# Kernel optimization log

Hardware: AMD Instinct MI355X
Metric: run time of the kernel (lower is better)

Reference implementation:

```python
import jax, jax.numpy as jnp
import numpy as np
import math

B, S, D, L, H, V, MAXP = 8, 512, 1024, 6, 8, 32000, 4096
HD = D // H
FF = 4 * D
EPS = 1e-5
SCALE = 1.0 / math.sqrt(HD)


def _ln(x, g, b):
    m = x.mean(-1, keepdims=True)
    xm = x - m
    v = (xm * xm).mean(-1, keepdims=True)
    return xm * jax.lax.rsqrt(v + EPS) * g + b


def setup_inputs() -> dict:
    key = jax.random.key(0)
    ks = jax.random.split(key, 16)
    std = 0.02
    inp = {
        'input_ids': jax.random.randint(ks[0], (B, S), 0, V, dtype=jnp.int32),
        'attention_mask': jnp.ones((B, S), dtype=jnp.int32),
        'current_position': 0,
        'tok_emb': jax.random.normal(ks[1], (V, D), jnp.float32) * std,
        'pos_emb': jax.random.normal(ks[2], (MAXP, D), jnp.float32) * std,
        'ln1_s': jnp.ones((L, D), jnp.float32),
        'ln1_b': jnp.zeros((L, D), jnp.float32),
        'Wq': jax.random.normal(ks[3], (L, D, D), jnp.float32) * std,
        'bq': jnp.zeros((L, D), jnp.float32),
        'Wk': jax.random.normal(ks[4], (L, D, D), jnp.float32) * std,
        'bk': jnp.zeros((L, D), jnp.float32),
        'Wv': jax.random.normal(ks[5], (L, D, D), jnp.float32) * std,
        'bv': jnp.zeros((L, D), jnp.float32),
        'Wo': jax.random.normal(ks[6], (L, D, D), jnp.float32) * std,
        'bo': jnp.zeros((L, D), jnp.float32),
        'ln2_s': jnp.ones((L, D), jnp.float32),
        'ln2_b': jnp.zeros((L, D), jnp.float32),
        'W1': jax.random.normal(ks[7], (L, D, FF), jnp.float32) * std,
        'b1': jnp.zeros((L, FF), jnp.float32),
        'W2': jax.random.normal(ks[8], (L, FF, D), jnp.float32) * std,
        'b2': jnp.zeros((L, D), jnp.float32),
        'lnf_s': jnp.ones((D,), jnp.float32),
        'lnf_b': jnp.zeros((D,), jnp.float32),
        'Wout': jax.random.normal(ks[9], (D, D), jnp.float32) * std,
        'bout': jnp.zeros((D,), jnp.float32),
    }
    return inp


def reference(input_ids, attention_mask, current_position, tok_emb, pos_emb,
              ln1_s, ln1_b, Wq, bq, Wk, bk, Wv, bv, Wo, bo,
              ln2_s, ln2_b, W1, b1, W2, b2, lnf_s, lnf_b, Wout, bout):
    pos = current_position + jnp.arange(S)  # [S]
    h = tok_emb[input_ids] + pos_emb[pos][None, :, :]  # [B,S,D]
    pad = (attention_mask == 0)[:, None, None, :]  # [B,1,1,S] key-padding mask

    def layer(h, p):
        (l1s, l1b, wq, bq_, wk, bk_, wv, bv_, wo, bo_,
         l2s, l2b, w1, b1_, w2, b2_) = p
        x = _ln(h, l1s, l1b)
        q = (x @ wq + bq_).reshape(B, S, H, HD).transpose(0, 2, 1, 3)
        k = (x @ wk + bk_).reshape(B, S, H, HD).transpose(0, 2, 1, 3)
        v = (x @ wv + bv_).reshape(B, S, H, HD).transpose(0, 2, 1, 3)
        scores = jnp.einsum('bhqd,bhkd->bhqk', q, k) * SCALE
        scores = jnp.where(pad, -10000.0, scores)
        attn = jax.nn.softmax(scores, axis=-1)
        o = jnp.einsum('bhqk,bhkd->bhqd', attn, v)
        o = o.transpose(0, 2, 1, 3).reshape(B, S, D)
        h = h + (o @ wo + bo_)
        x = _ln(h, l2s, l2b)
        mlp = jax.nn.gelu(x @ w1 + b1_, approximate=False) @ w2 + b2_
        return h + mlp, None

    h, _ = jax.lax.scan(layer, h, (ln1_s, ln1_b, Wq, bq, Wk, bk, Wv, bv, Wo, bo,
                                   ln2_s, ln2_b, W1, b1, W2, b2))
    h = _ln(h, lnf_s, lnf_b)
    return h @ Wout + bout
```

## Files before the change

kernel.cpp:

```cpp
#include <hip/hip_runtime.h>
#include <hip/hip_bf16.h>
#include <math.h>

#define BB 8
#define SS 512
#define DD 1024
#define LL 6
#define HH 8
#define HDD 128
#define FFF 4096
#define EPSF 1e-5f
#define SCALEF 0.08838834764831845f

typedef __attribute__((ext_vector_type(8))) _Float16 f16x8;
typedef __attribute__((ext_vector_type(4))) _Float16 f16x4;
typedef __attribute__((ext_vector_type(4))) float f32x4;

__device__ __forceinline__ void gload16(const void* g, void* l) {
  __builtin_amdgcn_global_load_lds(
      (const __attribute__((address_space(1))) void*)g,
      (__attribute__((address_space(3))) void*)l, 16, 0, 0);
}

__global__ __launch_bounds__(256, 3) void gemmk_kernel(
    const _Float16* __restrict__ Ag, const _Float16* __restrict__ Bg,
    const float* __restrict__ bias, void* __restrict__ outp,
    int Ndim, int Kdim, int Kstr, long zsA, long zsB, long zsOut, int emode) {
  __shared__ _Float16 lA[8192];
  __shared__ _Float16 lB[8192];
  const int tid = threadIdx.x;
  const int lane = tid & 63;
  const int wid = tid >> 6;
  const int z = blockIdx.z;
  const int m0 = blockIdx.y * 128;
  const int n0 = blockIdx.x * 128;
  const long K2 = (long)Kstr * 2;
  const _Float16* Az = Ag + (long)z * zsA + (long)m0 * Kstr;
  const _Float16* Bz = Bg + (long)z * zsB + (long)n0 * Kstr;

  const int wm = (wid >> 1) * 64;
  const int wn = (wid & 1) * 64;
  const int r16 = lane & 15;
  const int kq = lane >> 4;

  const char* As[4];
  const char* Bs[4];
  int ldd[4];
#pragma unroll
  for (int i = 0; i < 4; ++i) {
    const int idx = tid + i * 256;
    const int r = idx >> 3;
    const int sc = ((idx & 7) << 4) ^ ((r & 7) << 4);
    As[i] = (const char*)Az + (long)r * K2 + sc;
    Bs[i] = (const char*)Bz + (long)r * K2 + sc;
    ldd[i] = idx * 16;
  }

  f32x4 acc[4][4];
#pragma unroll
  for (int mi = 0; mi < 4; ++mi)
#pragma unroll
    for (int ni = 0; ni < 4; ++ni) acc[mi][ni] = (f32x4){0.f, 0.f, 0.f, 0.f};

  const int nt = Kdim >> 6;
  for (int t = 0; t < nt; ++t) {
    const int kb = t << 7;
    __syncthreads();
#pragma unroll
    for (int i = 0; i < 4; ++i) {
      gload16(As[i] + kb, (char*)lA + ldd[i]);
      gload16(Bs[i] + kb, (char*)lB + ldd[i]);
    }
    __syncthreads();
#pragma unroll
    for (int kk = 0; kk < 2; ++kk) {
      f16x8 af[4], bf[4];
#pragma unroll
      for (int mi = 0; mi < 4; ++mi) {
        const int R = wm + mi * 16 + r16;
        af[mi] = *(const f16x8*)((const char*)lA + R * 128 +
                                 ((kk * 64 + kq * 16) ^ ((R & 7) << 4)));
      }
#pragma unroll
      for (int ni = 0; ni < 4; ++ni) {
        const int R = wn + ni * 16 + r16;
        bf[ni] = *(const f16x8*)((const char*)lB + R * 128 +
                                 ((kk * 64 + kq * 16) ^ ((R & 7) << 4)));
      }
#pragma unroll
      for (int mi = 0; mi < 4; ++mi)
#pragma unroll
        for (int ni = 0; ni < 4; ++ni)
          acc[mi][ni] = __builtin_amdgcn_mfma_f32_16x16x32_f16(
              af[mi], bf[ni], acc[mi][ni], 0, 0, 0);
    }
  }

  _Float16* outH = (_Float16*)outp + (long)z * zsOut;
  const int rj = (lane >> 4) << 2;
  const long MSZq = (long)BB * SS * DD;
#pragma unroll
  for (int mi = 0; mi < 4; ++mi) {
#pragma unroll
    for (int ni = 0; ni < 4; ++ni) {
      const int col = n0 + wn + ni * 16 + r16;
#pragma unroll
      for (int j = 0; j < 4; ++j) {
        const int row = m0 + wm + mi * 16 + rj + j;
        float vv = acc[mi][ni][j];
        if (emode == 1) {
          vv += bias[col];
          int wsel = col >> 10, c = col & 1023;
          int b_ = row >> 9, s_ = row & 511;
          int hh = c >> 7, hd_ = c & 127;
          if (wsel < 2) {
            outH[wsel * MSZq + (((long)(b_ * HH + hh)) * SS + s_) * HDD + hd_] =
                (_Float16)vv;
          } else {
            outH[2 * MSZq + (((long)(b_ * HH + hh)) * HDD + hd_) * SS + s_] =
                (_Float16)vv;
          }
        } else if (emode == 5) {
          vv += bias[col];
          vv = 0.5f * vv * (1.0f + erff(vv * 0.70710678118654752f));
          outH[(long)row * Ndim + col] = (_Float16)vv;
        } else {
          outH[(long)row * Ndim + col] = (_Float16)vv;
        }
      }
    }
  }
}

__global__ __launch_bounds__(256) void flash_kernel(
    const _Float16* __restrict__ Qg, const _Float16* __restrict__ Kg,
    const _Float16* __restrict__ Vt, const int* __restrict__ amask,
    _Float16* __restrict__ xout) {
  __shared__ _Float16 Pl[4][32][136];
  __shared__ float rf_s[4][32];
  const int tid = threadIdx.x;
  const int lane = tid & 63;
  const int w = tid >> 6;
  const int bh = blockIdx.y;
  const int b_ = bh >> 3, hh = bh & 7;
  const int q0 = blockIdx.x * 128 + w * 32;
  const int r16 = lane & 15;
  const int kq = lane >> 4;
  const int rj = kq << 2;
  const _Float16* Qb = Qg + ((long)bh * SS + q0) * HDD;
  const _Float16* Kb = Kg + (long)bh * SS * HDD;
  const _Float16* Vb = Vt + (long)bh * HDD * SS;

  f16x8 qa[2][4];
#pragma unroll
  for (int mi = 0; mi < 2; ++mi)
#pragma unroll
    for (int kk = 0; kk < 4; ++kk)
      qa[mi][kk] = *(const f16x8*)(Qb + (long)(mi * 16 + r16) * HDD + kk * 32 +
                                   kq * 8);

  f32x4 acc[8][2];
#pragma unroll
  for (int mi = 0; mi < 8; ++mi)
#pragma unroll
    for (int ni = 0; ni < 2; ++ni) acc[mi][ni] = (f32x4){0.f, 0.f, 0.f, 0.f};
  float mrun[2][4], lrun[2][4];
#pragma unroll
  for (int mi = 0; mi < 2; ++mi)
#pragma unroll
    for (int j = 0; j < 4; ++j) {
      mrun[mi][j] = -INFINITY;
      lrun[mi][j] = 0.f;
    }

  for (int kt = 0; kt < 4; ++kt) {
    __syncthreads();
    const int s0 = kt * 128;
    int am[8];
#pragma unroll
    for (int ni = 0; ni < 8; ++ni)
      am[ni] = amask[b_ * SS + s0 + ni * 16 + r16];

    f32x4 sc[2][8];
#pragma unroll
    for (int mi = 0; mi < 2; ++mi)
#pragma unroll
      for (int ni = 0; ni < 8; ++ni) sc[mi][ni] = (f32x4){0.f, 0.f, 0.f, 0.f};
#pragma unroll
    for (int ni = 0; ni < 8; ++ni) {
      f16x8 kf[4];
#pragma unroll
      for (int kk = 0; kk < 4; ++kk)
        kf[kk] = *(const f16x8*)(Kb + (long)(s0 + ni * 16 + r16) * HDD +
                                 kk * 32 + kq * 8);
#pragma unroll
      for (int mi = 0; mi < 2; ++mi)
#pragma unroll
        for (int kk = 0; kk < 4; ++kk)
          sc[mi][ni] = __builtin_amdgcn_mfma_f32_16x16x32_f16(
              qa[mi][kk], kf[kk], sc[mi][ni], 0, 0, 0);
    }
#pragma unroll
    for (int mi = 0; mi < 2; ++mi)
#pragma unroll
      for (int ni = 0; ni < 8; ++ni)
#pragma unroll
        for (int j = 0; j < 4; ++j)
          sc[mi][ni][j] = am[ni] ? sc[mi][ni][j] * SCALEF : -10000.0f;

    float rf[2][4];
#pragma unroll
    for (int mi = 0; mi < 2; ++mi)
#pragma unroll
      for (int j = 0; j < 4; ++j) {
        float rm = -INFINITY;
#pragma unroll
        for (int ni = 0; ni < 8; ++ni) rm = fmaxf(rm, sc[mi][ni][j]);
#pragma unroll
        for (int off = 1; off < 16; off <<= 1)
          rm = fmaxf(rm, __shfl_xor(rm, off));
        const float mn = fmaxf(mrun[mi][j], rm);
        const float rfv = __expf(mrun[mi][j] - mn);
        mrun[mi][j] = mn;
        float rs = 0.f;
#pragma unroll
        for (int ni = 0; ni < 8; ++ni) {
          const float p = __expf(sc[mi][ni][j] - mn);
          sc[mi][ni][j] = p;
          rs += p;
        }
#pragma unroll
        for (int off = 1; off < 16; off <<= 1) rs += __shfl_xor(rs, off);
        lrun[mi][j] = lrun[mi][j] * rfv + rs;
        rf[mi][j] = rfv;
      }
    if (r16 == 0) {
#pragma unroll
      for (int mi = 0; mi < 2; ++mi)
#pragma unroll
        for (int j = 0; j < 4; ++j) rf_s[w][mi * 16 + rj + j] = rf[mi][j];
    }
#pragma unroll
    for (int mi = 0; mi < 2; ++mi)
#pragma unroll
      for (int ni = 0; ni < 8; ++ni)
#pragma unroll
        for (int j = 0; j < 4; ++j)
          Pl[w][mi * 16 + rj + j][ni * 16 + r16] = (_Float16)sc[mi][ni][j];
    __syncthreads();

    float rfq[2];
    rfq[0] = rf_s[w][r16];
    rfq[1] = rf_s[w][16 + r16];
#pragma unroll
    for (int mi2 = 0; mi2 < 8; ++mi2)
#pragma unroll
      for (int ni2 = 0; ni2 < 2; ++ni2)
#pragma unroll
        for (int j = 0; j < 4; ++j) acc[mi2][ni2][j] *= rfq[ni2];

    f16x8 pb[2][4];
#pragma unroll
    for (int ni2 = 0; ni2 < 2; ++ni2)
#pragma unroll
      for (int kk = 0; kk < 4; ++kk)
        pb[ni2][kk] =
            *(const f16x8*)(&Pl[w][ni2 * 16 + r16][kk * 32 + kq * 8]);
#pragma unroll
    for (int mi2 = 0; mi2 < 8; ++mi2) {
      f16x8 va[4];
#pragma unroll
      for (int kk = 0; kk < 4; ++kk)
        va[kk] = *(const f16x8*)(Vb + (long)(mi2 * 16 + r16) * SS + s0 +
                                 kk * 32 + kq * 8);
#pragma unroll
      for (int ni2 = 0; ni2 < 2; ++ni2)
#pragma unroll
        for (int kk = 0; kk < 4; ++kk)
          acc[mi2][ni2] = __builtin_amdgcn_mfma_f32_16x16x32_f16(
              va[kk], pb[ni2][kk], acc[mi2][ni2], 0, 0, 0);
    }
  }

  __syncthreads();
  if (r16 == 0) {
#pragma unroll
    for (int mi = 0; mi < 2; ++mi)
#pragma unroll
      for (int j = 0; j < 4; ++j)
        rf_s[w][mi * 16 + rj + j] = 1.0f / lrun[mi][j];
  }
  __syncthreads();
  float lq[2];
  lq[0] = rf_s[w][r16];
  lq[1] = rf_s[w][16 + r16];
#pragma unroll
  for (int mi2 = 0; mi2 < 8; ++mi2)
#pragma unroll
    for (int ni2 = 0; ni2 < 2; ++ni2) {
      f16x4 o;
#pragma unroll
      for (int j = 0; j < 4; ++j) o[j] = (_Float16)(acc[mi2][ni2][j] * lq[ni2]);
      const int qg = q0 + ni2 * 16 + r16;
      *(f16x4*)(&xout[((long)(b_ * SS + qg)) * DD + hh * HDD + mi2 * 16 + rj]) =
          o;
    }
}

__global__ __launch_bounds__(256) void reduce_ln_kernel(
    const _Float16* __restrict__ parts, int npart,
    const float* __restrict__ res, const float* __restrict__ bias,
    const float* __restrict__ lg, const float* __restrict__ lb,
    float* __restrict__ hout, _Float16* __restrict__ xout, long pzs) {
  const int row = blockIdx.x;
  const int c = threadIdx.x << 2;
  const long base = (long)row * DD + c;
  float4 a = *reinterpret_cast<const float4*>(&bias[c]);
  if (res) {
    const float4 r = *reinterpret_cast<const float4*>(&res[base]);
    a.x += r.x; a.y += r.y; a.z += r.z; a.w += r.w;
  }
  for (int p = 0; p < npart; ++p) {
    const f16x4 hpv = *reinterpret_cast<const f16x4*>(&parts[p * pzs + base]);
    a.x += (float)hpv[0]; a.y += (float)hpv[1];
    a.z += (float)hpv[2]; a.w += (float)hpv[3];
  }
  *reinterpret_cast<float4*>(&hout[base]) = a;
  if (!lg) return;
  float s = a.x + a.y + a.z + a.w;
  float ss = a.x * a.x + a.y * a.y + a.z * a.z + a.w * a.w;
#pragma unroll
  for (int off = 32; off; off >>= 1) {
    s += __shfl_down(s, off);
    ss += __shfl_down(ss, off);
  }
  __shared__ float red[8];
  const int wid = threadIdx.x >> 6, lane = threadIdx.x & 63;
  if (lane == 0) { red[wid] = s; red[4 + wid] = ss; }
  __syncthreads();
  if (threadIdx.x == 0) {
    s = red[0] + red[1] + red[2] + red[3];
    ss = red[4] + red[5] + red[6] + red[7];
    float mean = s * (1.0f / DD);
    float var = ss * (1.0f / DD) - mean * mean;
    red[0] = mean;
    red[1] = rsqrtf(var + EPSF);
  }
  __syncthreads();
  const float mean = red[0], rstd = red[1];
  const float4 gv = *reinterpret_cast<const float4*>(&lg[c]);
  const float4 bv = *reinterpret_cast<const float4*>(&lb[c]);
  f16x4 o;
  o[0] = (_Float16)((a.x - mean) * rstd * gv.x + bv.x);
  o[1] = (_Float16)((a.y - mean) * rstd * gv.y + bv.y);
  o[2] = (_Float16)((a.z - mean) * rstd * gv.z + bv.z);
  o[3] = (_Float16)((a.w - mean) * rstd * gv.w + bv.w);
  *reinterpret_cast<f16x4*>(&xout[base]) = o;
}

__global__ __launch_bounds__(256) void embed_ln_kernel(
    const int* __restrict__ ids, const int* __restrict__ curpos,
    const float* __restrict__ tok, const float* __restrict__ pos,
    const float* __restrict__ lg, const float* __restrict__ lb,
    float* __restrict__ h, _Float16* __restrict__ x) {
  const int rs = blockIdx.x;
  const int s_ = rs & (SS - 1);
  const int t = ids[rs];
  const int p = curpos[0] + s_;
  const int c = threadIdx.x << 2;
  const float4 tv = *reinterpret_cast<const float4*>(&tok[(long)t * DD + c]);
  const float4 pv = *reinterpret_cast<const float4*>(&pos[(long)p * DD + c]);
  float4 a = {tv.x + pv.x, tv.y + pv.y, tv.z + pv.z, tv.w + pv.w};
  *reinterpret_cast<float4*>(&h[(long)rs * DD + c]) = a;
  float s = a.x + a.y + a.z + a.w;
  float ss = a.x * a.x + a.y * a.y + a.z * a.z + a.w * a.w;
#pragma unroll
  for (int off = 32; off; off >>= 1) {
    s += __shfl_down(s, off);
    ss += __shfl_down(ss, off);
  }
  __shared__ float red[8];
  const int wid = threadIdx.x >> 6, lane = threadIdx.x & 63;
  if (lane == 0) { red[wid] = s; red[4 + wid] = ss; }
  __syncthreads();
  if (threadIdx.x == 0) {
    s = red[0] + red[1] + red[2] + red[3];
    ss = red[4] + red[5] + red[6] + red[7];
    float mean = s * (1.0f / DD);
    float var = ss * (1.0f / DD) - mean * mean;
    red[0] = mean;
    red[1] = rsqrtf(var + EPSF);
  }
  __syncthreads();
  const float mean = red[0], rstd = red[1];
  const float4 gv = *reinterpret_cast<const float4*>(&lg[c]);
  const float4 bv = *reinterpret_cast<const float4*>(&lb[c]);
  f16x4 o;
  o[0] = (_Float16)((a.x - mean) * rstd * gv.x + bv.x);
  o[1] = (_Float16)((a.y - mean) * rstd * gv.y + bv.y);
  o[2] = (_Float16)((a.z - mean) * rstd * gv.z + bv.z);
  o[3] = (_Float16)((a.w - mean) * rstd * gv.w + bv.w);
  *reinterpret_cast<f16x4*>(&x[(long)rs * DD + c]) = o;
}

__global__ __launch_bounds__(256) void wtransall_kernel(
    const float* __restrict__ Wq, const float* __restrict__ Wk,
    const float* __restrict__ Wv, const float* __restrict__ Wo,
    const float* __restrict__ W1, const float* __restrict__ W2, int l,
    _Float16* __restrict__ qkvT, _Float16* __restrict__ woT,
    _Float16* __restrict__ w1T, _Float16* __restrict__ w2T) {
  __shared__ float tt[64][65];
  const int id = blockIdx.x;
  const float* src;
  _Float16* dst;
  int K, N, t;
  const long lo = (long)l * DD * DD;
  const long lof = (long)l * DD * FFF;
  if (id < 1024) {
    const int wsel = id >> 8;
    t = id & 255;
    src = (wsel == 0 ? Wq : wsel == 1 ? Wk : wsel == 2 ? Wv : Wo) + lo;
    dst = (wsel < 3) ? (qkvT + (long)wsel * DD * DD) : woT;
    K = DD; N = DD;
  } else if (id < 2048) {
    t = id - 1024; src = W1 + lof; dst = w1T; K = DD; N = FFF;
  } else {
    t = id - 2048; src = W2 + lof; dst = w2T; K = FFF; N = DD;
  }
  const int ntile = N >> 6;
  const int n0 = (t % ntile) << 6;
  const int k0 = (t / ntile) << 6;
  const int tx = threadIdx.x & 63;
  const int ty = threadIdx.x >> 6;
#pragma unroll
  for (int i = 0; i < 16; ++i)
    tt[i * 4 + ty][tx] = src[(long)(k0 + i * 4 + ty) * N + n0 + tx];
  __syncthreads();
#pragma unroll
  for (int i = 0; i < 16; ++i) {
    const int r = i * 4 + ty;
    dst[(long)(n0 + r) * K + k0 + tx] = (_Float16)tt[tx][r];
  }
}

__global__ __launch_bounds__(256) void wtrans_kernel(
    const float* __restrict__ W, _Float16* __restrict__ WT, int K, int N) {
  __shared__ float tt[64][65];
  const int n0 = blockIdx.x * 64, k0 = blockIdx.y * 64;
  const int tx = threadIdx.x & 63;
  const int ty = threadIdx.x >> 6;
#pragma unroll
  for (int i = 0; i < 16; ++i)
    tt[i * 4 + ty][tx] = W[(long)(k0 + i * 4 + ty) * N + n0 + tx];
  __syncthreads();
#pragma unroll
  for (int i = 0; i < 16; ++i) {
    const int r = i * 4 + ty;
    WT[(long)(n0 + r) * K + k0 + tx] = (_Float16)tt[tx][r];
  }
}

__global__ __launch_bounds__(256) void packb_kernel(
    const float* __restrict__ bq, const float* __restrict__ bk,
    const float* __restrict__ bv, float* __restrict__ bqkv) {
  const int i = blockIdx.x * 256 + threadIdx.x;
  const int l = i / (3 * DD), j = i % (3 * DD);
  float v;
  if (j < DD) v = bq[l * DD + j];
  else if (j < 2 * DD) v = bk[l * DD + j - DD];
  else v = bv[l * DD + j - 2 * DD];
  bqkv[i] = v;
}

extern "C" void kernel_launch(void* const* d_in, const int* in_sizes, int n_in,
                              void* d_out, int out_size, void* d_ws,
                              size_t ws_size, hipStream_t stream) {
  const int* ids = (const int*)d_in[0];
  const int* amask = (const int*)d_in[1];
  const int* curp = (const int*)d_in[2];
  const float* tok = (const float*)d_in[3];
  const float* pose = (const float*)d_in[4];
  const float* ln1s = (const float*)d_in[5];
  const float* ln1b = (const float*)d_in[6];
  const float* Wq = (const float*)d_in[7];
  const float* bq = (const float*)d_in[8];
  const float* Wk = (const float*)d_in[9];
  const float* bk = (const float*)d_in[10];
  const float* Wv = (const float*)d_in[11];
  const float* bv = (const float*)d_in[12];
  const float* Wo = (const float*)d_in[13];
  const float* bo = (const float*)d_in[14];
  const float* ln2s = (const float*)d_in[15];
  const float* ln2b = (const float*)d_in[16];
  const float* W1 = (const float*)d_in[17];
  const float* b1 = (const float*)d_in[18];
  const float* W2 = (const float*)d_in[19];
  const float* b2 = (const float*)d_in[20];
  const float* lnfs = (const float*)d_in[21];
  const float* lnfb = (const float*)d_in[22];
  const float* Wout = (const float*)d_in[23];
  const float* bout = (const float*)d_in[24];

  const long MSZ = (long)BB * SS * DD;
  char* wsp = (char*)d_ws;
  float* h = (float*)wsp;
  _Float16* x = (_Float16*)(wsp + 16u * 1024 * 1024);
  _Float16* q = x + MSZ;
  _Float16* kb = q + MSZ;
  _Float16* vt = kb + MSZ;
  _Float16* big = vt + MSZ;
  _Float16* wqkvT = big + (long)BB * HH * SS * SS;
  _Float16* woT = wqkvT + 3L * DD * DD;
  _Float16* w1T = woT + (long)DD * DD;
  _Float16* w2T = w1T + (long)DD * FFF;
  float* bqkv = (float*)(w2T + (long)FFF * DD);
  _Float16* parts = (_Float16*)(bqkv + LL * 3 * DD);

  const int M = BB * SS;
  dim3 blk(256);
  const long pzs = (long)M * DD;

  embed_ln_kernel<<<M, blk, 0, stream>>>(ids, curp, tok, pose, ln1s, ln1b, h, x);
  packb_kernel<<<(LL * 3 * DD) / 256, blk, 0, stream>>>(bq, bk, bv, bqkv);

  const dim3 gQKV(3 * DD / 128, M / 128, 1);
  const dim3 gFA(SS / 128, BB * HH);
  const dim3 gF1(FFF / 128, M / 128, 1);
  const dim3 gK2(DD / 128, M / 128, 2);
  const dim3 gK4(DD / 128, M / 128, 4);
  const dim3 gWt(DD / 64, DD / 64);

  for (int l = 0; l < LL; ++l) {
    wtransall_kernel<<<3072, blk, 0, stream>>>(Wq, Wk, Wv, Wo, W1, W2, l,
                                               wqkvT, woT, w1T, w2T);
    gemmk_kernel<<<gQKV, blk, 0, stream>>>(x, wqkvT, bqkv + l * 3 * DD, q,
                                           3 * DD, DD, DD, 0, 0, 0, 1);
    flash_kernel<<<gFA, blk, 0, stream>>>(q, kb, vt, amask, x);
    gemmk_kernel<<<gK2, blk, 0, stream>>>(x, woT, nullptr, parts, DD, DD / 2,
                                          DD, DD / 2, DD / 2, pzs, 6);
    reduce_ln_kernel<<<M, blk, 0, stream>>>(parts, 2, h, bo + l * DD,
                                            ln2s + l * DD, ln2b + l * DD, h, x,
                                            pzs);
    gemmk_kernel<<<gF1, blk, 0, stream>>>(x, w1T, b1 + l * FFF, big, FFF, DD,
                                          DD, 0, 0, 0, 5);
    gemmk_kernel<<<gK4, blk, 0, stream>>>(big, w2T, nullptr, parts, DD,
                                          FFF / 4, FFF, FFF / 4, FFF / 4, pzs,
                                          6);
    const float* ng = (l < LL - 1) ? (ln1s + (l + 1) * DD) : lnfs;
    const float* nb = (l < LL - 1) ? (ln1b + (l + 1) * DD) : lnfb;
    reduce_ln_kernel<<<M, blk, 0, stream>>>(parts, 4, h, b2 + l * DD, ng, nb,
                                            h, x, pzs);
  }
  wtrans_kernel<<<gWt, blk, 0, stream>>>(Wout, woT, DD, DD);
  gemmk_kernel<<<gK2, blk, 0, stream>>>(x, woT, nullptr, parts, DD, DD / 2,
                                        DD, DD / 2, DD / 2, pzs, 6);
  reduce_ln_kernel<<<M, blk, 0, stream>>>(parts, 2, nullptr, bout, nullptr,
                                          nullptr, (float*)d_out, nullptr, pzs);
}
```

Measured before the change: 1.603 ms.

## Prepack all layer weights upfront, shrink flash tiles, split-K 4 for Wo

Transposes all six layers' weights into per-layer slabs with one launch up front when the workspace is large enough, instead of one transpose launch per layer. Flash attention now gives each wave 16 query rows instead of 32, which doubles the number of blocks and cuts register use. The Wo and output projections switch from split-K 2 to split-K 4, adding more partial sums for the reduce. The GEMM also raises its occupancy hint to 4 and recomputes load addresses to save registers. The risks are more K/V reloads per query row in attention and extra partial-sum traffic from the wider split-K.

New measurement: 1.732 ms. 1.08x slower.

```diff
diff --git a/kernel.cpp b/kernel.cpp
--- a/kernel.cpp
+++ b/kernel.cpp
@@ -22,7 +22,7 @@
       (__attribute__((address_space(3))) void*)l, 16, 0, 0);
 }
 
-__global__ __launch_bounds__(256, 3) void gemmk_kernel(
+__global__ __launch_bounds__(256, 4) void gemmk_kernel(
     const _Float16* __restrict__ Ag, const _Float16* __restrict__ Bg,
     const float* __restrict__ bias, void* __restrict__ outp,
     int Ndim, int Kdim, int Kstr, long zsA, long zsB, long zsOut, int emode) {
@@ -35,25 +35,21 @@
   const int m0 = blockIdx.y * 128;
   const int n0 = blockIdx.x * 128;
   const long K2 = (long)Kstr * 2;
-  const _Float16* Az = Ag + (long)z * zsA + (long)m0 * Kstr;
-  const _Float16* Bz = Bg + (long)z * zsB + (long)n0 * Kstr;
+  const char* Azc = (const char*)(Ag + (long)z * zsA + (long)m0 * Kstr);
+  const char* Bzc = (const char*)(Bg + (long)z * zsB + (long)n0 * Kstr);
 
   const int wm = (wid >> 1) * 64;
   const int wn = (wid & 1) * 64;
   const int r16 = lane & 15;
   const int kq = lane >> 4;
 
-  const char* As[4];
-  const char* Bs[4];
-  int ldd[4];
+  long roff[4];
 #pragma unroll
   for (int i = 0; i < 4; ++i) {
     const int idx = tid + i * 256;
     const int r = idx >> 3;
     const int sc = ((idx & 7) << 4) ^ ((r & 7) << 4);
-    As[i] = (const char*)Az + (long)r * K2 + sc;
-    Bs[i] = (const char*)Bz + (long)r * K2 + sc;
-    ldd[i] = idx * 16;
+    roff[i] = (long)r * K2 + sc;
   }
 
   f32x4 acc[4][4];
@@ -68,8 +64,8 @@
     __syncthreads();
 #pragma unroll
     for (int i = 0; i < 4; ++i) {
-      gload16(As[i] + kb, (char*)lA + ldd[i]);
-      gload16(Bs[i] + kb, (char*)lB + ldd[i]);
+      gload16(Azc + roff[i] + kb, (char*)lA + tid * 16 + i * 4096);
+      gload16(Bzc + roff[i] + kb, (char*)lB + tid * 16 + i * 4096);
     }
     __syncthreads();
 #pragma unroll
@@ -136,14 +132,14 @@
     const _Float16* __restrict__ Qg, const _Float16* __restrict__ Kg,
     const _Float16* __restrict__ Vt, const int* __restrict__ amask,
     _Float16* __restrict__ xout) {
-  __shared__ _Float16 Pl[4][32][136];
-  __shared__ float rf_s[4][32];
+  __shared__ _Float16 Pl[4][16][136];
+  __shared__ float rf_s[4][16];
   const int tid = threadIdx.x;
   const int lane = tid & 63;
   const int w = tid >> 6;
   const int bh = blockIdx.y;
   const int b_ = bh >> 3, hh = bh & 7;
-  const int q0 = blockIdx.x * 128 + w * 32;
+  const int q0 = blockIdx.x * 64 + w * 16;
   const int r16 = lane & 15;
   const int kq = lane >> 4;
   const int rj = kq << 2;
@@ -151,27 +147,20 @@
   const _Float16* Kb = Kg + (long)bh * SS * HDD;
   const _Float16* Vb = Vt + (long)bh * HDD * SS;
 
-  f16x8 qa[2][4];
-#pragma unroll
-  for (int mi = 0; mi < 2; ++mi)
-#pragma unroll
-    for (int kk = 0; kk < 4; ++kk)
-      qa[mi][kk] = *(const f16x8*)(Qb + (long)(mi * 16 + r16) * HDD + kk * 32 +
-                                   kq * 8);
-
-  f32x4 acc[8][2];
-#pragma unroll
-  for (int mi = 0; mi < 8; ++mi)
-#pragma unroll
-    for (int ni = 0; ni < 2; ++ni) acc[mi][ni] = (f32x4){0.f, 0.f, 0.f, 0.f};
-  float mrun[2][4], lrun[2][4];
-#pragma unroll
-  for (int mi = 0; mi < 2; ++mi)
-#pragma unroll
-    for (int j = 0; j < 4; ++j) {
-      mrun[mi][j] = -INFINITY;
-      lrun[mi][j] = 0.f;
-    }
+  f16x8 qa[4];
+#pragma unroll
+  for (int kk = 0; kk < 4; ++kk)
+    qa[kk] = *(const f16x8*)(Qb + (long)r16 * HDD + kk * 32 + kq * 8);
+
+  f32x4 acc[8];
+#pragma unroll
+  for (int mi = 0; mi < 8; ++mi) acc[mi] = (f32x4){0.f, 0.f, 0.f, 0.f};
+  float mrun[4], lrun[4];
+#pragma unroll
+  for (int j = 0; j < 4; ++j) {
+    mrun[j] = -INFINITY;
+    lrun[j] = 0.f;
+  }
 
   for (int kt = 0; kt < 4; ++kt) {
     __syncthreads();
@@ -181,11 +170,9 @@
     for (int ni = 0; ni < 8; ++ni)
       am[ni] = amask[b_ * SS + s0 + ni * 16 + r16];
 
-    f32x4 sc[2][8];
-#pragma unroll
-    for (int mi = 0; mi < 2; ++mi)
-#pragma unroll
-      for (int ni = 0; ni < 8; ++ni) sc[mi][ni] = (f32x4){0.f, 0.f, 0.f, 0.f};
+    f32x4 sc[8];
+#pragma unroll
+    for (int ni = 0; ni < 8; ++ni) sc[ni] = (f32x4){0.f, 0.f, 0.f, 0.f};
 #pragma unroll
     for (int ni = 0; ni < 8; ++ni) {
       f16x8 kf[4];
@@ -194,117 +181,89 @@
         kf[kk] = *(const f16x8*)(Kb + (long)(s0 + ni * 16 + r16) * HDD +
                                  kk * 32 + kq * 8);
 #pragma unroll
-      for (int mi = 0; mi < 2; ++mi)
-#pragma unroll
-        for (int kk = 0; kk < 4; ++kk)
-          sc[mi][ni] = __builtin_amdgcn_mfma_f32_16x16x32_f16(
-              qa[mi][kk], kf[kk], sc[mi][ni], 0, 0, 0);
-    }
-#pragma unroll
-    for (int mi = 0; mi < 2; ++mi)
-#pragma unroll
-      for (int ni = 0; ni < 8; ++ni)
-#pragma unroll
-        for (int j = 0; j < 4; ++j)
-          sc[mi][ni][j] = am[ni] ? sc[mi][ni][j] * SCALEF : -10000.0f;
-
-    float rf[2][4];
-#pragma unroll
-    for (int mi = 0; mi < 2; ++mi)
-#pragma unroll
-      for (int j = 0; j < 4; ++j) {
-        float rm = -INFINITY;
-#pragma unroll
-        for (int ni = 0; ni < 8; ++ni) rm = fmaxf(rm, sc[mi][ni][j]);
-#pragma unroll
-        for (int off = 1; off < 16; off <<= 1)
-          rm = fmaxf(rm, __shfl_xor(rm, off));
-        const float mn = fmaxf(mrun[mi][j], rm);
-        const float rfv = __expf(mrun[mi][j] - mn);
-        mrun[mi][j] = mn;
-        float rs = 0.f;
-#pragma unroll
-        for (int ni = 0; ni < 8; ++ni) {
-          const float p = __expf(sc[mi][ni][j] - mn);
-          sc[mi][ni][j] = p;
-          rs += p;
-        }
-#pragma unroll
-        for (int off = 1; off < 16; off <<= 1) rs += __shfl_xor(rs, off);
-        lrun[mi][j] = lrun[mi][j] * rfv + rs;
-        rf[mi][j] = rfv;
+      for (int kk = 0; kk < 4; ++kk)
+        sc[ni] = __builtin_amdgcn_mfma_f32_16x16x32_f16(qa[kk], kf[kk], sc[ni],
+                                                        0, 0, 0);
+    }
+#pragma unroll
+    for (int ni = 0; ni < 8; ++ni)
+#pragma unroll
+      for (int j = 0; j < 4; ++j)
+        sc[ni][j] = am[ni] ? sc[ni][j] * SCALEF : -10000.0f;
+
+    float rf[4];
+#pragma unroll
+    for (int j = 0; j < 4; ++j) {
+      float rm = -INFINITY;
+#pragma unroll
+      for (int ni = 0; ni < 8; ++ni) rm = fmaxf(rm, sc[ni][j]);
+#pragma unroll
+      for (int off = 1; off < 16; off <<= 1) rm = fmaxf(rm, __shfl_xor(rm, off));
+      const float mn = fmaxf(mrun[j], rm);
+      const float rfv = __expf(mrun[j] - mn);
+      mrun[j] = mn;
+      float rs = 0.f;
+#pragma unroll
+      for (int ni = 0; ni < 8; ++ni) {
+        const float p = __expf(sc[ni][j] - mn);
+        sc[ni][j] = p;
+        rs += p;
       }
+#pragma unroll
+      for (int off = 1; off < 16; off <<= 1) rs += __shfl_xor(rs, off);
+      lrun[j] = lrun[j] * rfv + rs;
+      rf[j] = rfv;
+    }
     if (r16 == 0) {
 #pragma unroll
-      for (int mi = 0; mi < 2; ++mi)
-#pragma unroll
-        for (int j = 0; j < 4; ++j) rf_s[w][mi * 16 + rj + j] = rf[mi][j];
-    }
-#pragma unroll
-    for (int mi = 0; mi < 2; ++mi)
-#pragma unroll
-      for (int ni = 0; ni < 8; ++ni)
-#pragma unroll
-        for (int j = 0; j < 4; ++j)
-          Pl[w][mi * 16 + rj + j][ni * 16 + r16] = (_Float16)sc[mi][ni][j];
+      for (int j = 0; j < 4; ++j) rf_s[w][rj + j] = rf[j];
+    }
+#pragma unroll
+    for (int ni = 0; ni < 8; ++ni)
+#pragma unroll
+      for (int j = 0; j < 4; ++j)
+        Pl[w][rj + j][ni * 16 + r16] = (_Float16)sc[ni][j];
     __syncthreads();
 
-    float rfq[2];
-    rfq[0] = rf_s[w][r16];
-    rfq[1] = rf_s[w][16 + r16];
-#pragma unroll
-    for (int mi2 = 0; mi2 < 8; ++mi2)
-#pragma unroll
-      for (int ni2 = 0; ni2 < 2; ++ni2)
-#pragma unroll
-        for (int j = 0; j < 4; ++j) acc[mi2][ni2][j] *= rfq[ni2];
-
-    f16x8 pb[2][4];
-#pragma unroll
-    for (int ni2 = 0; ni2 < 2; ++ni2)
+    const float rfq = rf_s[w][r16];
+#pragma unroll
+    for (int mi = 0; mi < 8; ++mi)
+#pragma unroll
+      for (int j = 0; j < 4; ++j) acc[mi][j] *= rfq;
+
+    f16x8 pb[4];
+#pragma unroll
+    for (int kk = 0; kk < 4; ++kk)
+      pb[kk] = *(const f16x8*)(&Pl[w][r16][kk * 32 + kq * 8]);
+#pragma unroll
+    for (int mi = 0; mi < 8; ++mi) {
+      f16x8 va[4];
 #pragma unroll
       for (int kk = 0; kk < 4; ++kk)
-        pb[ni2][kk] =
-            *(const f16x8*)(&Pl[w][ni2 * 16 + r16][kk * 32 + kq * 8]);
-#pragma unroll
-    for (int mi2 = 0; mi2 < 8; ++mi2) {
-      f16x8 va[4];
+        va[kk] = *(const f16x8*)(Vb + (long)(mi * 16 + r16) * SS + s0 +
+                                 kk * 32 + kq * 8);
 #pragma unroll
       for (int kk = 0; kk < 4; ++kk)
-        va[kk] = *(const f16x8*)(Vb + (long)(mi2 * 16 + r16) * SS + s0 +
-                                 kk * 32 + kq * 8);
-#pragma unroll
-      for (int ni2 = 0; ni2 < 2; ++ni2)
-#pragma unroll
-        for (int kk = 0; kk < 4; ++kk)
-          acc[mi2][ni2] = __builtin_amdgcn_mfma_f32_16x16x32_f16(
-              va[kk], pb[ni2][kk], acc[mi2][ni2], 0, 0, 0);
+        acc[mi] = __builtin_amdgcn_mfma_f32_16x16x32_f16(va[kk], pb[kk],
+                                                         acc[mi], 0, 0, 0);
     }
   }
 
   __syncthreads();
   if (r16 == 0) {
 #pragma unroll
-    for (int mi = 0; mi < 2; ++mi)
-#pragma unroll
-      for (int j = 0; j < 4; ++j)
-        rf_s[w][mi * 16 + rj + j] = 1.0f / lrun[mi][j];
-  }
-  __syncthreads();
-  float lq[2];
-  lq[0] = rf_s[w][r16];
-  lq[1] = rf_s[w][16 + r16];
-#pragma unroll
-  for (int mi2 = 0; mi2 < 8; ++mi2)
-#pragma unroll
-    for (int ni2 = 0; ni2 < 2; ++ni2) {
-      f16x4 o;
-#pragma unroll
-      for (int j = 0; j < 4; ++j) o[j] = (_Float16)(acc[mi2][ni2][j] * lq[ni2]);
-      const int qg = q0 + ni2 * 16 + r16;
-      *(f16x4*)(&xout[((long)(b_ * SS + qg)) * DD + hh * HDD + mi2 * 16 + rj]) =
-          o;
-    }
+    for (int j = 0; j < 4; ++j) rf_s[w][rj + j] = 1.0f / lrun[j];
+  }
+  __syncthreads();
+  const float lq = rf_s[w][r16];
+#pragma unroll
+  for (int mi = 0; mi < 8; ++mi) {
+    f16x4 o;
+#pragma unroll
+    for (int j = 0; j < 4; ++j) o[j] = (_Float16)(acc[mi][j] * lq);
+    *(f16x4*)(&xout[((long)(b_ * SS + q0 + r16)) * DD + hh * HDD + mi * 16 +
+                    rj]) = o;
+  }
 }
 
 __global__ __launch_bounds__(256) void reduce_ln_kernel(
@@ -403,29 +362,33 @@
   *reinterpret_cast<f16x4*>(&x[(long)rs * DD + c]) = o;
 }
 
+#define SLABE 12582912L
 __global__ __launch_bounds__(256) void wtransall_kernel(
     const float* __restrict__ Wq, const float* __restrict__ Wk,
     const float* __restrict__ Wv, const float* __restrict__ Wo,
-    const float* __restrict__ W1, const float* __restrict__ W2, int l,
-    _Float16* __restrict__ qkvT, _Float16* __restrict__ woT,
-    _Float16* __restrict__ w1T, _Float16* __restrict__ w2T) {
+    const float* __restrict__ W1, const float* __restrict__ W2, int lbase,
+    long slabstride, _Float16* __restrict__ wall) {
   __shared__ float tt[64][65];
   const int id = blockIdx.x;
+  const int lrel = id / 3072;
+  const int l = lbase + lrel;
+  int t = id % 3072;
+  _Float16* slab = wall + (long)lrel * slabstride;
+  const long lo = (long)l * DD * DD;
+  const long lof = (long)l * DD * FFF;
   const float* src;
   _Float16* dst;
-  int K, N, t;
-  const long lo = (long)l * DD * DD;
-  const long lof = (long)l * DD * FFF;
-  if (id < 1024) {
-    const int wsel = id >> 8;
-    t = id & 255;
+  int K, N;
+  if (t < 1024) {
+    const int wsel = t >> 8;
+    t &= 255;
     src = (wsel == 0 ? Wq : wsel == 1 ? Wk : wsel == 2 ? Wv : Wo) + lo;
-    dst = (wsel < 3) ? (qkvT + (long)wsel * DD * DD) : woT;
+    dst = (wsel < 3) ? (slab + (long)wsel * DD * DD) : (slab + 3L * DD * DD);
     K = DD; N = DD;
-  } else if (id < 2048) {
-    t = id - 1024; src = W1 + lof; dst = w1T; K = DD; N = FFF;
+  } else if (t < 2048) {
+    t -= 1024; src = W1 + lof; dst = slab + 4L * DD * DD; K = DD; N = FFF;
   } else {
-    t = id - 2048; src = W2 + lof; dst = w2T; K = FFF; N = DD;
+    t -= 2048; src = W2 + lof; dst = slab + 8L * DD * DD; K = FFF; N = DD;
   }
   const int ntile = N >> 6;
   const int n0 = (t % ntile) << 6;
@@ -509,12 +472,14 @@
   _Float16* kb = q + MSZ;
   _Float16* vt = kb + MSZ;
   _Float16* big = vt + MSZ;
-  _Float16* wqkvT = big + (long)BB * HH * SS * SS;
-  _Float16* woT = wqkvT + 3L * DD * DD;
-  _Float16* w1T = woT + (long)DD * DD;
-  _Float16* w2T = w1T + (long)DD * FFF;
-  float* bqkv = (float*)(w2T + (long)FFF * DD);
-  _Float16* parts = (_Float16*)(bqkv + LL * 3 * DD);
+  _Float16* parts = big + MSZ * 4;
+  float* bqkv = (float*)(parts + MSZ * 4);
+  _Float16* wall = (_Float16*)((char*)bqkv + 128 * 1024);
+  const size_t base_b = (size_t)((char*)wall - wsp);
+  const bool prepack =
+      ws_size >= base_b + (size_t)(6 * SLABE + (long)DD * DD) * 2 + 4096;
+  const int nslab = prepack ? 6 : 1;
+  _Float16* woutT = wall + (long)nslab * SLABE;
 
   const int M = BB * SS;
   dim3 blk(256);
@@ -522,23 +487,31 @@
 
   embed_ln_kernel<<<M, blk, 0, stream>>>(ids, curp, tok, pose, ln1s, ln1b, h, x);
   packb_kernel<<<(LL * 3 * DD) / 256, blk, 0, stream>>>(bq, bk, bv, bqkv);
+  wtrans_kernel<<<dim3(DD / 64, DD / 64), blk, 0, stream>>>(Wout, woutT, DD, DD);
+  if (prepack)
+    wtransall_kernel<<<6 * 3072, blk, 0, stream>>>(Wq, Wk, Wv, Wo, W1, W2, 0,
+                                                   SLABE, wall);
 
   const dim3 gQKV(3 * DD / 128, M / 128, 1);
-  const dim3 gFA(SS / 128, BB * HH);
+  const dim3 gFA(SS / 64, BB * HH);
   const dim3 gF1(FFF / 128, M / 128, 1);
-  const dim3 gK2(DD / 128, M / 128, 2);
   const dim3 gK4(DD / 128, M / 128, 4);
-  const dim3 gWt(DD / 64, DD / 64);
 
   for (int l = 0; l < LL; ++l) {
-    wtransall_kernel<<<3072, blk, 0, stream>>>(Wq, Wk, Wv, Wo, W1, W2, l,
-                                               wqkvT, woT, w1T, w2T);
-    gemmk_kernel<<<gQKV, blk, 0, stream>>>(x, wqkvT, bqkv + l * 3 * DD, q,
+    _Float16* slab = wall + (long)(prepack ? l : 0) * SLABE;
+    _Float16* qkvT = slab;
+    _Float16* woT = slab + 3L * DD * DD;
+    _Float16* w1T = slab + 4L * DD * DD;
+    _Float16* w2T = slab + 8L * DD * DD;
+    if (!prepack)
+      wtransall_kernel<<<3072, blk, 0, stream>>>(Wq, Wk, Wv, Wo, W1, W2, l, 0,
+                                                 wall);
+    gemmk_kernel<<<gQKV, blk, 0, stream>>>(x, qkvT, bqkv + l * 3 * DD, q,
                                            3 * DD, DD, DD, 0, 0, 0, 1);
     flash_kernel<<<gFA, blk, 0, stream>>>(q, kb, vt, amask, x);
-    gemmk_kernel<<<gK2, blk, 0, stream>>>(x, woT, nullptr, parts, DD, DD / 2,
-                                          DD, DD / 2, DD / 2, pzs, 6);
-    reduce_ln_kernel<<<M, blk, 0, stream>>>(parts, 2, h, bo + l * DD,
+    gemmk_kernel<<<gK4, blk, 0, stream>>>(x, woT, nullptr, parts, DD, DD / 4,
+                                          DD, DD / 4, DD / 4, pzs, 6);
+    reduce_ln_kernel<<<M, blk, 0, stream>>>(parts, 4, h, bo + l * DD,
                                             ln2s + l * DD, ln2b + l * DD, h, x,
                                             pzs);
     gemmk_kernel<<<gF1, blk, 0, stream>>>(x, w1T, b1 + l * FFF, big, FFF, DD,
@@ -551,9 +524,8 @@
     reduce_ln_kernel<<<M, blk, 0, stream>>>(parts, 4, h, b2 + l * DD, ng, nb,
                                             h, x, pzs);
   }
-  wtrans_kernel<<<gWt, blk, 0, stream>>>(Wout, woT, DD, DD);
-  gemmk_kernel<<<gK2, blk, 0, stream>>>(x, woT, nullptr, parts, DD, DD / 2,
-                                        DD, DD / 2, DD / 2, pzs, 6);
-  reduce_ln_kernel<<<M, blk, 0, stream>>>(parts, 2, nullptr, bout, nullptr,
+  gemmk_kernel<<<gK4, blk, 0, stream>>>(x, woutT, nullptr, parts, DD, DD / 4,
+                                        DD, DD / 4, DD / 4, pzs, 6);
+  reduce_ln_kernel<<<M, blk, 0, stream>>>(parts, 4, nullptr, bout, nullptr,
                                           nullptr, (float*)d_out, nullptr, pzs);
 }
```
